# Kernel optimization log

Hardware: AMD Instinct MI355X
Metric: run time of the kernel (lower is better)

## Reference

```python
import jax, jax.numpy as jnp
import numpy as np

B, N, HID = 4, 16384, 512
H, M = 8, 32          # num_heads, num_slices
D = HID // H          # head_dim = 64


def setup_inputs() -> dict:
    key = jax.random.key(0)
    ks = jax.random.split(key, 8)
    std = 0.02
    return {
        "x": jax.random.normal(ks[0], (B, N, HID), jnp.float32),
        # Linear weights stored as [in, out] (y = x @ W + b)
        "wkv_w": jax.random.normal(ks[1], (HID, 2 * HID), jnp.float32) * std,
        "wkv_b": jnp.zeros((2 * HID,), jnp.float32),
        "wtq": jax.random.normal(ks[2], (H, M, D), jnp.float32) * std,
        "alpha": jnp.ones((H,), jnp.float32),
        "qkv_w": jax.random.normal(ks[3], (HID, 3 * HID), jnp.float32) * std,
        "out_w": jax.random.normal(ks[4], (HID, HID), jnp.float32) * std,
        "out_b": jnp.zeros((HID,), jnp.float32),
    }


def _split_heads(t):  # [b, n, h*d] -> [b, h, n, d]
    b, n, _ = t.shape
    return t.reshape(b, n, H, D).transpose(0, 2, 1, 3)


def _mha(q, k, v):
    scale = q.shape[-1] ** -0.5
    dots = jnp.einsum('bhqd,bhkd->bhqk', q, k) * scale
    attn = jax.nn.softmax(dots, axis=-1)
    out = jnp.einsum('bhqk,bhkd->bhqd', attn, v)
    return out, attn


def reference(x, wkv_w, wkv_b, wtq, alpha, qkv_w, out_w, out_b):
    kv = x @ wkv_w + wkv_b                      # [b, n, 2*hid]
    xk, xv = kv[..., :HID], kv[..., HID:]
    xk = _split_heads(xk)                       # [b, h, n, d]
    xv = _split_heads(xv)

    # slot/slice cross-attention: softmax over the slice axis m (axis=-2)
    slice_scores = jnp.einsum('hmd,bhnd->bhmn', wtq, xk)
    slice_weights = jax.nn.softmax(slice_scores * alpha[None, :, None, None], axis=-2)
    slice_token = jnp.einsum('bhmn,bhnd->bhmd', slice_weights, xv)
    slice_token = slice_token / (slice_weights.sum(axis=-1, keepdims=True) + 1e-5)
    slice_token = slice_token.transpose(0, 2, 1, 3).reshape(B, M, HID)  # b m (h d)

    # small inner MHA over the m=32 slices
    qkv = slice_token @ qkv_w                   # [b, m, 3*hid]
    q_t = _split_heads(qkv[..., :HID])
    k_t = _split_heads(qkv[..., HID:2 * HID])
    v_t = _split_heads(qkv[..., 2 * HID:])
    out_token, attn_weights = _mha(q_t, k_t, v_t)

    # scatter slice outputs back to n positions
    out = jnp.einsum('bhmd,bhmn->bhnd', out_token, slice_weights)
    out = out.transpose(0, 2, 1, 3).reshape(B, N, HID)  # b n (h d)
    out = out @ out_w + out_b
    return out, slice_weights, alpha, jnp.zeros((H, M), jnp.float32), attn_weights
```

## Files before the change

### kernel.cpp

```cpp
#include <hip/hip_runtime.h>

#define B_ 4
#define N_ 16384
#define HID_ 512
#define H_ 8
#define M_ 32
#define D_ 64

typedef __attribute__((ext_vector_type(8))) short short8;
typedef __attribute__((ext_vector_type(4))) float f32x4;

__device__ __forceinline__ short f2bf(float f) {
    unsigned u = __float_as_uint(f);
    u += 0x7fffu + ((u >> 16) & 1u);
    return (short)(u >> 16);
}
__device__ __forceinline__ float bf2f(short s) {
    return __uint_as_float(((unsigned)(unsigned short)s) << 16);
}
__device__ __forceinline__ unsigned pack2(float a, float b) {
    return (unsigned)(unsigned short)f2bf(a) | ((unsigned)(unsigned short)f2bf(b) << 16);
}
__device__ __forceinline__ void gl_lds16(const short* g, short* l) {
    __builtin_amdgcn_global_load_lds((const __attribute__((address_space(1))) unsigned*)g,
                                     (__attribute__((address_space(3))) unsigned*)l, 16, 0, 0);
}

__global__ void k_misc(const float* __restrict__ alpha, float* __restrict__ a_out,
                       float* __restrict__ z_out, const float* __restrict__ wtq,
                       short* __restrict__ wtq_bf) {
    int i = blockIdx.x * 256 + threadIdx.x;
    wtq_bf[i] = f2bf(wtq[i]);
    if (blockIdx.x == 0) {
        int t = threadIdx.x;
        if (t < H_) a_out[t] = alpha[t];
        z_out[t] = 0.f;
    }
}

__global__ void k_cvt(const float* __restrict__ src, short* __restrict__ dst) {
    int i = blockIdx.x * 256 + threadIdx.x;
    const f32x4* s = (const f32x4*)(src) + (size_t)i * 2;
    f32x4 a = s[0], b = s[1];
    short8 o;
    o[0] = f2bf(a[0]); o[1] = f2bf(a[1]); o[2] = f2bf(a[2]); o[3] = f2bf(a[3]);
    o[4] = f2bf(b[0]); o[5] = f2bf(b[1]); o[6] = f2bf(b[2]); o[7] = f2bf(b[3]);
    ((short8*)dst)[i] = o;
}

__global__ __launch_bounds__(256)
void k_wt(const float* __restrict__ w, short* __restrict__ wt) {
    __shared__ float ls[64][65];
    const int t = threadIdx.x;
    const int n0 = blockIdx.x * 64, k0 = blockIdx.y * 64;
#pragma unroll
    for (int p = 0; p < 16; ++p) {
        int idx = p * 256 + t;
        int kk = idx >> 6, nn = idx & 63;
        ls[kk][nn] = w[(size_t)(k0 + kk) * 1024 + n0 + nn];
    }
    __syncthreads();
#pragma unroll
    for (int p = 0; p < 16; ++p) {
        int idx = p * 256 + t;
        int nn = idx >> 6, kk = idx & 63;
        wt[(size_t)(n0 + nn) * 512 + k0 + kk] = f2bf(ls[kk][nn]);
    }
}

template <bool OUT_BF16>
__global__ __launch_bounds__(256, 2)
void mfma_gemm(const short* __restrict__ A, const short* __restrict__ Bt,
               const float* __restrict__ bias, void* __restrict__ Cv,
               int K, int Ncols, int b_stride, int rows_per_b, int lgx) {
    __shared__ short As[128 * 32];
    __shared__ short Bs[128 * 32];
    const int t = threadIdx.x;
    const int nwg = gridDim.x * gridDim.y;
    int id = blockIdx.y * gridDim.x + blockIdx.x;
    id = (id & 7) * (nwg >> 3) + (id >> 3);
    const int col0 = (id & ((1 << lgx) - 1)) * 128;
    const int row0 = (id >> lgx) * 128;
    const short* Bblk = Bt;
    if (b_stride) Bblk += (size_t)(row0 / rows_per_b) * (size_t)b_stride;

    const int r_a = t >> 2;
    const int c_a = (t & 3) << 3;
    const short* Ap = A + (size_t)(row0 + r_a) * K + c_a;
    const short* Bp = Bblk + (size_t)(col0 + r_a) * K + c_a;
    short* As0 = &As[t << 3];
    short* Bs0 = &Bs[t << 3];
    const size_t rowskip = (size_t)64 * K;

    const int w = t >> 6;
    const int L = t & 63;
    const int wm = (w >> 1) << 6;
    const int wn = (w & 1) << 6;
    const int lm = L & 15;
    const int lq = L >> 4;

    f32x4 acc[4][4];
#pragma unroll
    for (int i = 0; i < 4; ++i)
#pragma unroll
        for (int j = 0; j < 4; ++j) acc[i][j] = (f32x4){0.f, 0.f, 0.f, 0.f};

    for (int k0 = 0; k0 < K; k0 += 32) {
        gl_lds16(Ap + k0, As0);
        gl_lds16(Ap + k0 + rowskip, As0 + 2048);
        gl_lds16(Bp + k0, Bs0);
        gl_lds16(Bp + k0 + rowskip, Bs0 + 2048);
        __syncthreads();
        short8 af[4], bfr[4];
#pragma unroll
        for (int i = 0; i < 4; ++i)
            af[i] = *(const short8*)&As[((wm + (i << 4) + lm) << 5) + (lq << 3)];
#pragma unroll
        for (int j = 0; j < 4; ++j)
            bfr[j] = *(const short8*)&Bs[((wn + (j << 4) + lm) << 5) + (lq << 3)];
#pragma unroll
        for (int i = 0; i < 4; ++i)
#pragma unroll
            for (int j = 0; j < 4; ++j)
                acc[i][j] = __builtin_amdgcn_mfma_f32_16x16x32_bf16(af[i], bfr[j], acc[i][j], 0, 0, 0);
        __syncthreads();
    }
#pragma unroll
    for (int i = 0; i < 4; ++i) {
#pragma unroll
        for (int j = 0; j < 4; ++j) {
            const int gr = row0 + wm + (i << 4) + (lq << 2);
            const int gc = col0 + wn + (j << 4) + lm;
            const float bv = bias[gc];
#pragma unroll
            for (int r = 0; r < 4; ++r) {
                float v = acc[i][j][r] + bv;
                if constexpr (OUT_BF16)
                    ((short*)Cv)[(size_t)(gr + r) * Ncols + gc] = f2bf(v);
                else
                    ((float*)Cv)[(size_t)(gr + r) * Ncols + gc] = v;
            }
        }
    }
}

__global__ __launch_bounds__(256, 4)
void k_score(const short* __restrict__ kv, const short* __restrict__ wtq_bf,
             const float* __restrict__ alpha, float* __restrict__ sw_out,
             float* __restrict__ pws) {
    const int t = threadIdx.x;
    const int bx = blockIdx.x;
    const int chunk = bx & 63;
    const int h = (bx >> 6) & 7;
    const int b = bx >> 9;
    const int w = t >> 6;
    const int L = t & 63;
    const int lm = L & 15;
    const int g = L >> 4;
    const int n0 = chunk * 256;
    const size_t rowb = (size_t)(b * N_ + n0);
    const float al = alpha[h];

    short8 bq[2][2];
    const short* wq = wtq_bf + h * (M_ * D_);
#pragma unroll
    for (int mt = 0; mt < 2; ++mt)
#pragma unroll
        for (int ks = 0; ks < 2; ++ks)
            bq[mt][ks] = *(const short8*)(wq + (mt * 16 + lm) * 64 + ks * 32 + g * 8);

    f32x4 s[4][2];
#pragma unroll
    for (int nt = 0; nt < 4; ++nt)
#pragma unroll
        for (int mt = 0; mt < 2; ++mt) s[nt][mt] = (f32x4){0.f, 0.f, 0.f, 0.f};
#pragma unroll
    for (int ks = 0; ks < 2; ++ks) {
        short8 aq[4];
#pragma unroll
        for (int nt = 0; nt < 4; ++nt)
            aq[nt] = *(const short8*)(kv + (rowb + w * 64 + nt * 16 + lm) * 1024 +
                                      h * 64 + ks * 32 + g * 8);
#pragma unroll
        for (int nt = 0; nt < 4; ++nt)
#pragma unroll
            for (int mt = 0; mt < 2; ++mt)
                s[nt][mt] = __builtin_amdgcn_mfma_f32_16x16x32_bf16(aq[nt], bq[mt][ks], s[nt][mt], 0, 0, 0);
    }

#pragma unroll
    for (int nt = 0; nt < 4; ++nt)
#pragma unroll
        for (int r = 0; r < 4; ++r) {
            float v0 = s[nt][0][r] * al, v1 = s[nt][1][r] * al;
            float mx = fmaxf(v0, v1);
#pragma unroll
            for (int d2 = 1; d2 < 16; d2 <<= 1) mx = fmaxf(mx, __shfl_xor(mx, d2));
            float e0 = __expf(v0 - mx), e1 = __expf(v1 - mx);
            float sm = e0 + e1;
#pragma unroll
            for (int d2 = 1; d2 < 16; d2 <<= 1) sm += __shfl_xor(sm, d2);
            float inv = 1.f / sm;
            s[nt][0][r] = e0 * inv;
            s[nt][1][r] = e1 * inv;
        }

    float ws0 = 0.f, ws1 = 0.f;
#pragma unroll
    for (int nt = 0; nt < 4; ++nt) {
        const int nn = w * 64 + nt * 16 + g * 4;
#pragma unroll
        for (int mt = 0; mt < 2; ++mt) {
            const int m = mt * 16 + lm;
            *(f32x4*)(sw_out + ((size_t)((b * 8 + h) * 32 + m)) * N_ + n0 + nn) = s[nt][mt];
            float w4 = s[nt][mt][0] + s[nt][mt][1] + s[nt][mt][2] + s[nt][mt][3];
            if (mt == 0) ws0 += w4; else ws1 += w4;
        }
    }
    ws0 += __shfl_xor(ws0, 16); ws0 += __shfl_xor(ws0, 32);
    ws1 += __shfl_xor(ws1, 16); ws1 += __shfl_xor(ws1, 32);
    if (L < 16) {
        float* pw = pws + (((size_t)((b * 8 + h) * 64 + chunk)) * 4 + w) * 32;
        pw[lm] = ws0;
        pw[16 + lm] = ws1;
    }
}

__global__ __attribute__((amdgpu_flat_work_group_size(256, 256), amdgpu_waves_per_eu(3, 3)))
void k_wsum(const short* __restrict__ kv, const float* __restrict__ sw_out,
            short* __restrict__ swT, float* __restrict__ pnum) {
    __shared__ __attribute__((aligned(16))) short wT_s[M_ * 256];
    __shared__ __attribute__((aligned(16))) short xvT_s[D_ * 256];
    const int t = threadIdx.x;
    const int bx = blockIdx.x;
    const int chunk = bx & 63;
    const int h = (bx >> 6) & 7;
    const int b = bx >> 9;
    const int w = t >> 6;
    const int L = t & 63;
    const int lm = L & 15;
    const int g = L >> 4;
    const int n0 = chunk * 256;
    const size_t rowb = (size_t)(b * N_ + n0);

    short8 xv8[8];
    const short8* xvp = (const short8*)(kv + (rowb + t) * 1024 + HID_ + h * 64);
#pragma unroll
    for (int i = 0; i < 8; ++i) xv8[i] = xvp[i];

    {
        const int m = t >> 3, i = t & 7;
        const int xr = (m & 7) << 3;
        const float* rp = sw_out + ((size_t)((b * 8 + h) * 32 + m)) * N_ + n0 + i * 32;
#pragma unroll
        for (int q = 0; q < 4; ++q) {
            f32x4 a = ((const f32x4*)rp)[2 * q];
            f32x4 c = ((const f32x4*)rp)[2 * q + 1];
            int nn = i * 32 + q * 8;
            short8 v;
            v[0] = f2bf(a[0]); v[1] = f2bf(a[1]); v[2] = f2bf(a[2]); v[3] = f2bf(a[3]);
            v[4] = f2bf(c[0]); v[5] = f2bf(c[1]); v[6] = f2bf(c[2]); v[7] = f2bf(c[3]);
            *(short8*)(wT_s + m * 256 + (nn ^ xr)) = v;
        }
    }

#pragma unroll
    for (int i = 0; i < 8; ++i)
#pragma unroll
        for (int j = 0; j < 8; ++j)
            xvT_s[(i * 8 + j) * 256 + (t ^ (j << 3))] = xv8[i][j];

    __syncthreads();

    const int dcol = w * 16 + lm;
    f32x4 acc2[2];
    acc2[0] = (f32x4){0.f, 0.f, 0.f, 0.f};
    acc2[1] = (f32x4){0.f, 0.f, 0.f, 0.f};
#pragma unroll
    for (int ks = 0; ks < 8; ++ks) {
        const int kb = ks * 32 + g * 8;
        short8 bv = *(const short8*)(xvT_s + dcol * 256 + (kb ^ ((lm & 7) << 3)));
#pragma unroll
        for (int mt = 0; mt < 2; ++mt) {
            const int m = mt * 16 + lm;
            short8 av = *(const short8*)(wT_s + m * 256 + (kb ^ ((lm & 7) << 3)));
            acc2[mt] = __builtin_amdgcn_mfma_f32_16x16x32_bf16(av, bv, acc2[mt], 0, 0, 0);
        }
    }

    {
        unsigned pk[16];
#pragma unroll
        for (int mp = 0; mp < 16; ++mp) {
            unsigned a0 = (unsigned short)wT_s[(2 * mp) * 256 + (t ^ (((2 * mp) & 7) << 3))];
            unsigned a1 = (unsigned short)wT_s[(2 * mp + 1) * 256 + (t ^ (((2 * mp + 1) & 7) << 3))];
            pk[mp] = a0 | (a1 << 16);
        }
        short8* swtp = (short8*)(swT + (rowb + t) * 256 + h * 32);
#pragma unroll
        for (int q = 0; q < 4; ++q) {
            short8 v;
            v[0] = (short)(pk[4 * q] & 0xffff);     v[1] = (short)(pk[4 * q] >> 16);
            v[2] = (short)(pk[4 * q + 1] & 0xffff); v[3] = (short)(pk[4 * q + 1] >> 16);
            v[4] = (short)(pk[4 * q + 2] & 0xffff); v[5] = (short)(pk[4 * q + 2] >> 16);
            v[6] = (short)(pk[4 * q + 3] & 0xffff); v[7] = (short)(pk[4 * q + 3] >> 16);
            swtp[q] = v;
        }
    }

    float* pn = pnum + ((size_t)((b * 8 + h) * 64 + chunk)) * 2048;
#pragma unroll
    for (int mt = 0; mt < 2; ++mt)
#pragma unroll
        for (int r = 0; r < 4; ++r)
            pn[(mt * 16 + g * 4 + r) * 64 + dcol] = acc2[mt][r];
}

__global__ __launch_bounds__(256)
void k_reduce(const float* __restrict__ pnum, const float* __restrict__ pws,
              float* __restrict__ num, float* __restrict__ wsum) {
    const int bid = blockIdx.x, t = threadIdx.x;
    if (bid < 256) {
        int e = bid * 256 + t;
        int bh = e >> 11, md = e & 2047;
        const float* p = pnum + (size_t)bh * 64 * 2048 + md;
        float s = 0.f;
#pragma unroll 4
        for (int c = 0; c < 64; ++c) s += p[c * 2048];
        num[e] = s;
    } else {
        int e = (bid - 256) * 256 + t;
        int bh = e >> 5, m = e & 31;
        const float* p = pws + (size_t)bh * 64 * 4 * 32 + m;
        float s = 0.f;
#pragma unroll 4
        for (int cw = 0; cw < 256; ++cw) s += p[cw * 32];
        wsum[e] = s;
    }
}

__global__ __launch_bounds__(256, 2)
void k_qkv(const float* __restrict__ num, const float* __restrict__ wsum,
           const float* __restrict__ qkv_w, float* __restrict__ qkv) {
    __shared__ float st_s[512 * 32];
    const int t = threadIdx.x;
    const int b = blockIdx.y;
    for (int p = 0; p < 64; ++p) {
        int idx = p * 256 + t;
        int m = idx & 31, k = idx >> 5;
        int h = k >> 6, d = k & 63;
        float wsv = wsum[(b * H_ + h) * M_ + m];
        st_s[k * 32 + m] = num[((size_t)(b * H_ + h) * M_ + m) * 64 + d] / (wsv + 1e-5f);
    }
    __syncthreads();
    const int m = t >> 3;
    const int c0 = blockIdx.x * 64 + (t & 7) * 8;
    float acc[8] = {};
    for (int k = 0; k < 512; ++k) {
        float sv = st_s[k * 32 + m];
        const f32x4* wp = (const f32x4*)(qkv_w + (size_t)k * 1536 + c0);
        f32x4 w0 = wp[0], w1 = wp[1];
        acc[0] += sv * w0[0]; acc[1] += sv * w0[1]; acc[2] += sv * w0[2]; acc[3] += sv * w0[3];
        acc[4] += sv * w1[0]; acc[5] += sv * w1[1]; acc[6] += sv * w1[2]; acc[7] += sv * w1[3];
    }
    float* dst = qkv + (size_t)(b * M_ + m) * 1536 + c0;
#pragma unroll
    for (int i = 0; i < 8; ++i) dst[i] = acc[i];
}

__global__ __launch_bounds__(256)
void k_mha(const float* __restrict__ qkv, float* __restrict__ attn_out,
           float* __restrict__ ot) {
    __shared__ float q_s[32 * 65], k_s[32 * 65], v_s[32 * 65];
    __shared__ float s_s[32 * 33], p_s[32 * 33];
    const int bx = blockIdx.x;
    const int b = bx >> 3, h = bx & 7;
    const int t = threadIdx.x;
    for (int p = 0; p < 8; ++p) {
        int idx = p * 256 + t;
        int m = idx >> 6, d = idx & 63;
        size_t base = (size_t)(b * M_ + m) * 1536 + h * 64 + d;
        q_s[m * 65 + d] = qkv[base];
        k_s[m * 65 + d] = qkv[base + 512];
        v_s[m * 65 + d] = qkv[base + 1024];
    }
    __syncthreads();
    for (int p = 0; p < 4; ++p) {
        int c = p * 256 + t;
        int m = c >> 5, mm = c & 31;
        float a = 0.f;
#pragma unroll
        for (int d = 0; d < 64; ++d) a += q_s[m * 65 + d] * k_s[mm * 65 + d];
        s_s[m * 33 + mm] = a * 0.125f;
    }
    __syncthreads();
    if (t < 32) {
        float mx = -1e30f;
        for (int mm = 0; mm < 32; ++mm) mx = fmaxf(mx, s_s[t * 33 + mm]);
        float sum = 0.f;
        for (int mm = 0; mm < 32; ++mm) {
            float e = __expf(s_s[t * 33 + mm] - mx);
            p_s[t * 33 + mm] = e;
            sum += e;
        }
        float inv = 1.f / sum;
        for (int mm = 0; mm < 32; ++mm) {
            float av = p_s[t * 33 + mm] * inv;
            p_s[t * 33 + mm] = av;
            attn_out[((size_t)(b * H_ + h) * M_ + t) * M_ + mm] = av;
        }
    }
    __syncthreads();
    const int m = t >> 3, d0 = (t & 7) * 8;
    float acc[8] = {};
    for (int mm = 0; mm < 32; ++mm) {
        float av = p_s[m * 33 + mm];
#pragma unroll
        for (int j = 0; j < 8; ++j) acc[j] += av * v_s[mm * 65 + d0 + j];
    }
    float* dst = ot + ((size_t)(b * H_ + h) * M_ + m) * 64 + d0;
#pragma unroll
    for (int j = 0; j < 8; ++j) dst[j] = acc[j];
}

__global__ __launch_bounds__(256)
void k_p(const float* __restrict__ ot, const float* __restrict__ out_w,
         short* __restrict__ Pt) {
    __shared__ float ot_s[32 * 65];
    const int bh = blockIdx.y;
    const int b = bh >> 3, h = bh & 7;
    const int t = threadIdx.x;
    for (int p = 0; p < 8; ++p) {
        int idx = p * 256 + t;
        int m = idx >> 6, d = idx & 63;
        ot_s[m * 65 + d] = ot[(size_t)bh * (M_ * 64) + idx];
    }
    __syncthreads();
    const int j = blockIdx.x * 128 + (t & 127);
    const int mh = (t >> 7) * 16;
    float acc[16] = {};
    for (int d = 0; d < 64; ++d) {
        float ow = out_w[(size_t)(h * 64 + d) * HID_ + j];
#pragma unroll
        for (int i = 0; i < 16; ++i) acc[i] += ot_s[(mh + i) * 65 + d] * ow;
    }
    short* dst = Pt + ((size_t)b * HID_ + j) * (H_ * M_) + h * M_ + mh;
#pragma unroll
    for (int i = 0; i < 16; i += 2) *(unsigned*)(dst + i) = pack2(acc[i], acc[i + 1]);
}

extern "C" void kernel_launch(void* const* d_in, const int* in_sizes, int n_in,
                              void* d_out, int out_size, void* d_ws, size_t ws_size,
                              hipStream_t stream) {
    const float* x     = (const float*)d_in[0];
    const float* wkv_w = (const float*)d_in[1];
    const float* wkv_b = (const float*)d_in[2];
    const float* wtq   = (const float*)d_in[3];
    const float* alpha = (const float*)d_in[4];
    const float* qkv_w = (const float*)d_in[5];
    const float* out_w = (const float*)d_in[6];
    const float* out_b = (const float*)d_in[7];

    float* out       = (float*)d_out;
    float* sw_out    = out + (size_t)B_ * N_ * HID_;
    float* alpha_out = sw_out + (size_t)B_ * H_ * M_ * N_;
    float* zeros_out = alpha_out + H_;
    float* attn_out  = zeros_out + H_ * M_;

    short* x_bf = (short*)sw_out;
    float* pnum = out;
    float* pws  = out + 4194304;

    char* ws = (char*)d_ws;
    short* kv   = (short*)(ws);
    short* swT  = (short*)(ws + 134217728);
    short* wkvT = (short*)(ws + 167772160);
    short* Pt   = (short*)(ws + 168820736);
    float* num  = (float*)(ws + 169869312);
    float* wsum = (float*)(ws + 170131456);
    float* qkvb = (float*)(ws + 170135552);
    float* ot   = (float*)(ws + 170921984);
    short* wtq_bf = (short*)(ws + 170921984);

    k_misc<<<64, 256, 0, stream>>>(alpha, alpha_out, zeros_out, wtq, wtq_bf);
    k_cvt<<<16384, 256, 0, stream>>>(x, x_bf);
    k_wt<<<dim3(16, 8), 256, 0, stream>>>(wkv_w, wkvT);
    mfma_gemm<true><<<dim3(8, 512), 256, 0, stream>>>(
        x_bf, wkvT, wkv_b, (void*)kv, 512, 1024, 0, 1 << 30, 3);
    k_score<<<2048, 256, 0, stream>>>(kv, wtq_bf, alpha, sw_out, pws);
    k_wsum<<<2048, 256, 0, stream>>>(kv, sw_out, swT, pnum);
    k_reduce<<<260, 256, 0, stream>>>(pnum, pws, num, wsum);
    k_qkv<<<dim3(24, 4), 256, 0, stream>>>(num, wsum, qkv_w, qkvb);
    k_mha<<<32, 256, 0, stream>>>(qkvb, attn_out, ot);
    k_p<<<dim3(4, 32), 256, 0, stream>>>(ot, out_w, Pt);
    mfma_gemm<false><<<dim3(4, 512), 256, 0, stream>>>(
        swT, Pt, out_b, (void*)out, 256, 512, 131072, 16384, 2);
}
```

Baseline: 571.5 us.

## Fuse slice-score softmax into KV projection GEMM epilogue, drop K materialization

New measurement: 607.2 us. 1.06x slower.

```diff
diff --git a/kernel.cpp b/kernel.cpp
--- a/kernel.cpp
+++ b/kernel.cpp
@@ -68,6 +68,172 @@
     }
 }
 
+__global__ __launch_bounds__(256, 2)
+void k_kv(const short* __restrict__ A, const short* __restrict__ Bt,
+          const float* __restrict__ bias, const short* __restrict__ wtq_bf,
+          const float* __restrict__ alpha, short* __restrict__ vout,
+          float* __restrict__ sw_out, float* __restrict__ pws) {
+    __shared__ short As[128 * 32];
+    __shared__ short Bs[128 * 32];
+    __shared__ short Ss[128 * 128];
+    const int t = threadIdx.x;
+    int id = blockIdx.y * 8 + blockIdx.x;
+    id = (id & 7) * 512 + (id >> 3);
+    const int xb = id & 7;
+    const int row0 = (id >> 3) * 128;
+    const int col0 = xb * 128;
+    const int K = 512;
+
+    const int r_a = t >> 2;
+    const int c_a = (t & 3) << 3;
+    const short* Ap = A + (size_t)(row0 + r_a) * K + c_a;
+    const short* Bp = Bt + (size_t)(col0 + r_a) * K + c_a;
+    short* As0 = &As[t << 3];
+    short* Bs0 = &Bs[t << 3];
+    const size_t rowskip = (size_t)64 * K;
+
+    const int w = t >> 6;
+    const int L = t & 63;
+    const int wm = (w >> 1) << 6;
+    const int wn = (w & 1) << 6;
+    const int lm = L & 15;
+    const int lq = L >> 4;
+
+    f32x4 acc[4][4];
+#pragma unroll
+    for (int i = 0; i < 4; ++i)
+#pragma unroll
+        for (int j = 0; j < 4; ++j) acc[i][j] = (f32x4){0.f, 0.f, 0.f, 0.f};
+
+    for (int k0 = 0; k0 < K; k0 += 32) {
+        gl_lds16(Ap + k0, As0);
+        gl_lds16(Ap + k0 + rowskip, As0 + 2048);
+        gl_lds16(Bp + k0, Bs0);
+        gl_lds16(Bp + k0 + rowskip, Bs0 + 2048);
+        __syncthreads();
+        short8 af[4], bfr[4];
+#pragma unroll
+        for (int i = 0; i < 4; ++i)
+            af[i] = *(const short8*)&As[((wm + (i << 4) + lm) << 5) + (lq << 3)];
+#pragma unroll
+        for (int j = 0; j < 4; ++j)
+            bfr[j] = *(const short8*)&Bs[((wn + (j << 4) + lm) << 5) + (lq << 3)];
+#pragma unroll
+        for (int i = 0; i < 4; ++i)
+#pragma unroll
+            for (int j = 0; j < 4; ++j)
+                acc[i][j] = __builtin_amdgcn_mfma_f32_16x16x32_bf16(af[i], bfr[j], acc[i][j], 0, 0, 0);
+        __syncthreads();
+    }
+
+    if (xb >= 4) {
+        const int vc0 = col0 - 512;
+#pragma unroll
+        for (int i = 0; i < 4; ++i) {
+#pragma unroll
+            for (int j = 0; j < 4; ++j) {
+                const int gr = row0 + wm + (i << 4) + (lq << 2);
+                const int cl = wn + (j << 4) + lm;
+                const float bv = bias[col0 + cl];
+#pragma unroll
+                for (int r = 0; r < 4; ++r)
+                    vout[(size_t)(gr + r) * 512 + vc0 + cl] = f2bf(acc[i][j][r] + bv);
+            }
+        }
+        return;
+    }
+
+#pragma unroll
+    for (int i = 0; i < 4; ++i) {
+#pragma unroll
+        for (int j = 0; j < 4; ++j) {
+            const int cl = wn + (j << 4) + lm;
+            const float bv = bias[col0 + cl];
+#pragma unroll
+            for (int r = 0; r < 4; ++r) {
+                const int tok = wm + (i << 4) + (lq << 2) + r;
+                Ss[tok * 128 + (cl ^ ((tok & 7) << 3))] = f2bf(acc[i][j][r] + bv);
+            }
+        }
+    }
+    __syncthreads();
+
+    const int b = row0 >> 14;
+    const int nb = row0 & 16383;
+    const int panel = nb >> 7;
+    const int g = lq;
+#pragma unroll
+    for (int hh = 0; hh < 2; ++hh) {
+        const int hg = 2 * xb + hh;
+        const float al = alpha[hg];
+        const short* wq = wtq_bf + hg * (M_ * D_);
+        short8 bq[2][2];
+#pragma unroll
+        for (int mt = 0; mt < 2; ++mt)
+#pragma unroll
+            for (int ks = 0; ks < 2; ++ks)
+                bq[mt][ks] = *(const short8*)(wq + (mt * 16 + lm) * 64 + ks * 32 + g * 8);
+
+        f32x4 sc[2][2];
+#pragma unroll
+        for (int nt = 0; nt < 2; ++nt)
+#pragma unroll
+            for (int mt = 0; mt < 2; ++mt) sc[nt][mt] = (f32x4){0.f, 0.f, 0.f, 0.f};
+#pragma unroll
+        for (int ks = 0; ks < 2; ++ks) {
+            short8 aq[2];
+#pragma unroll
+            for (int nt = 0; nt < 2; ++nt) {
+                const int tok = w * 32 + nt * 16 + lm;
+                const int chan = hh * 64 + ks * 32 + g * 8;
+                aq[nt] = *(const short8*)&Ss[tok * 128 + (chan ^ ((tok & 7) << 3))];
+            }
+#pragma unroll
+            for (int nt = 0; nt < 2; ++nt)
+#pragma unroll
+                for (int mt = 0; mt < 2; ++mt)
+                    sc[nt][mt] = __builtin_amdgcn_mfma_f32_16x16x32_bf16(aq[nt], bq[mt][ks], sc[nt][mt], 0, 0, 0);
+        }
+
+#pragma unroll
+        for (int nt = 0; nt < 2; ++nt)
+#pragma unroll
+            for (int r = 0; r < 4; ++r) {
+                float v0 = sc[nt][0][r] * al, v1 = sc[nt][1][r] * al;
+                float mx = fmaxf(v0, v1);
+#pragma unroll
+                for (int d2 = 1; d2 < 16; d2 <<= 1) mx = fmaxf(mx, __shfl_xor(mx, d2));
+                float e0 = __expf(v0 - mx), e1 = __expf(v1 - mx);
+                float sm = e0 + e1;
+#pragma unroll
+                for (int d2 = 1; d2 < 16; d2 <<= 1) sm += __shfl_xor(sm, d2);
+                float inv = 1.f / sm;
+                sc[nt][0][r] = e0 * inv;
+                sc[nt][1][r] = e1 * inv;
+            }
+
+        float ws0 = 0.f, ws1 = 0.f;
+#pragma unroll
+        for (int nt = 0; nt < 2; ++nt) {
+            const int nn = nb + w * 32 + nt * 16 + g * 4;
+#pragma unroll
+            for (int mt = 0; mt < 2; ++mt) {
+                const int m = mt * 16 + lm;
+                *(f32x4*)(sw_out + ((size_t)((b * 8 + hg) * 32 + m)) * N_ + nn) = sc[nt][mt];
+                float w4 = sc[nt][mt][0] + sc[nt][mt][1] + sc[nt][mt][2] + sc[nt][mt][3];
+                if (mt == 0) ws0 += w4; else ws1 += w4;
+            }
+        }
+        ws0 += __shfl_xor(ws0, 16); ws0 += __shfl_xor(ws0, 32);
+        ws1 += __shfl_xor(ws1, 16); ws1 += __shfl_xor(ws1, 32);
+        if (L < 16) {
+            float* pw = pws + (((size_t)((b * 8 + hg) * 128 + panel)) * 4 + w) * 32;
+            pw[lm] = ws0;
+            pw[16 + lm] = ws1;
+        }
+    }
+}
+
 template <bool OUT_BF16>
 __global__ __launch_bounds__(256, 2)
 void mfma_gemm(const short* __restrict__ A, const short* __restrict__ Bt,
@@ -144,10 +310,11 @@
     }
 }
 
-__global__ __launch_bounds__(256, 4)
-void k_score(const short* __restrict__ kv, const short* __restrict__ wtq_bf,
-             const float* __restrict__ alpha, float* __restrict__ sw_out,
-             float* __restrict__ pws) {
+__global__ __attribute__((amdgpu_flat_work_group_size(256, 256), amdgpu_waves_per_eu(3, 3)))
+void k_wsum(const short* __restrict__ v, const float* __restrict__ sw_out,
+            short* __restrict__ swT, float* __restrict__ pnum) {
+    __shared__ __attribute__((aligned(16))) short wT_s[M_ * 256];
+    __shared__ __attribute__((aligned(16))) short xvT_s[D_ * 256];
     const int t = threadIdx.x;
     const int bx = blockIdx.x;
     const int chunk = bx & 63;
@@ -159,92 +326,9 @@
     const int g = L >> 4;
     const int n0 = chunk * 256;
     const size_t rowb = (size_t)(b * N_ + n0);
-    const float al = alpha[h];
-
-    short8 bq[2][2];
-    const short* wq = wtq_bf + h * (M_ * D_);
-#pragma unroll
-    for (int mt = 0; mt < 2; ++mt)
-#pragma unroll
-        for (int ks = 0; ks < 2; ++ks)
-            bq[mt][ks] = *(const short8*)(wq + (mt * 16 + lm) * 64 + ks * 32 + g * 8);
-
-    f32x4 s[4][2];
-#pragma unroll
-    for (int nt = 0; nt < 4; ++nt)
-#pragma unroll
-        for (int mt = 0; mt < 2; ++mt) s[nt][mt] = (f32x4){0.f, 0.f, 0.f, 0.f};
-#pragma unroll
-    for (int ks = 0; ks < 2; ++ks) {
-        short8 aq[4];
-#pragma unroll
-        for (int nt = 0; nt < 4; ++nt)
-            aq[nt] = *(const short8*)(kv + (rowb + w * 64 + nt * 16 + lm) * 1024 +
-                                      h * 64 + ks * 32 + g * 8);
-#pragma unroll
-        for (int nt = 0; nt < 4; ++nt)
-#pragma unroll
-            for (int mt = 0; mt < 2; ++mt)
-                s[nt][mt] = __builtin_amdgcn_mfma_f32_16x16x32_bf16(aq[nt], bq[mt][ks], s[nt][mt], 0, 0, 0);
-    }
-
-#pragma unroll
-    for (int nt = 0; nt < 4; ++nt)
-#pragma unroll
-        for (int r = 0; r < 4; ++r) {
-            float v0 = s[nt][0][r] * al, v1 = s[nt][1][r] * al;
-            float mx = fmaxf(v0, v1);
-#pragma unroll
-            for (int d2 = 1; d2 < 16; d2 <<= 1) mx = fmaxf(mx, __shfl_xor(mx, d2));
-            float e0 = __expf(v0 - mx), e1 = __expf(v1 - mx);
-            float sm = e0 + e1;
-#pragma unroll
-            for (int d2 = 1; d2 < 16; d2 <<= 1) sm += __shfl_xor(sm, d2);
-            float inv = 1.f / sm;
-            s[nt][0][r] = e0 * inv;
-            s[nt][1][r] = e1 * inv;
-        }
-
-    float ws0 = 0.f, ws1 = 0.f;
-#pragma unroll
-    for (int nt = 0; nt < 4; ++nt) {
-        const int nn = w * 64 + nt * 16 + g * 4;
-#pragma unroll
-        for (int mt = 0; mt < 2; ++mt) {
-            const int m = mt * 16 + lm;
-            *(f32x4*)(sw_out + ((size_t)((b * 8 + h) * 32 + m)) * N_ + n0 + nn) = s[nt][mt];
-            float w4 = s[nt][mt][0] + s[nt][mt][1] + s[nt][mt][2] + s[nt][mt][3];
-            if (mt == 0) ws0 += w4; else ws1 += w4;
-        }
-    }
-    ws0 += __shfl_xor(ws0, 16); ws0 += __shfl_xor(ws0, 32);
-    ws1 += __shfl_xor(ws1, 16); ws1 += __shfl_xor(ws1, 32);
-    if (L < 16) {
-        float* pw = pws + (((size_t)((b * 8 + h) * 64 + chunk)) * 4 + w) * 32;
-        pw[lm] = ws0;
-        pw[16 + lm] = ws1;
-    }
-}
-
-__global__ __attribute__((amdgpu_flat_work_group_size(256, 256), amdgpu_waves_per_eu(3, 3)))
-void k_wsum(const short* __restrict__ kv, const float* __restrict__ sw_out,
-            short* __restrict__ swT, float* __restrict__ pnum) {
-    __shared__ __attribute__((aligned(16))) short wT_s[M_ * 256];
-    __shared__ __attribute__((aligned(16))) short xvT_s[D_ * 256];
-    const int t = threadIdx.x;
-    const int bx = blockIdx.x;
-    const int chunk = bx & 63;
-    const int h = (bx >> 6) & 7;
-    const int b = bx >> 9;
-    const int w = t >> 6;
-    const int L = t & 63;
-    const int lm = L & 15;
-    const int g = L >> 4;
-    const int n0 = chunk * 256;
-    const size_t rowb = (size_t)(b * N_ + n0);
 
     short8 xv8[8];
-    const short8* xvp = (const short8*)(kv + (rowb + t) * 1024 + HID_ + h * 64);
+    const short8* xvp = (const short8*)(v + (rowb + t) * 512 + h * 64);
 #pragma unroll
     for (int i = 0; i < 8; ++i) xv8[i] = xvp[i];
 
@@ -257,10 +341,10 @@
             f32x4 a = ((const f32x4*)rp)[2 * q];
             f32x4 c = ((const f32x4*)rp)[2 * q + 1];
             int nn = i * 32 + q * 8;
-            short8 v;
-            v[0] = f2bf(a[0]); v[1] = f2bf(a[1]); v[2] = f2bf(a[2]); v[3] = f2bf(a[3]);
-            v[4] = f2bf(c[0]); v[5] = f2bf(c[1]); v[6] = f2bf(c[2]); v[7] = f2bf(c[3]);
-            *(short8*)(wT_s + m * 256 + (nn ^ xr)) = v;
+            short8 vv;
+            vv[0] = f2bf(a[0]); vv[1] = f2bf(a[1]); vv[2] = f2bf(a[2]); vv[3] = f2bf(a[3]);
+            vv[4] = f2bf(c[0]); vv[5] = f2bf(c[1]); vv[6] = f2bf(c[2]); vv[7] = f2bf(c[3]);
+            *(short8*)(wT_s + m * 256 + (nn ^ xr)) = vv;
         }
     }
 
@@ -299,12 +383,12 @@
         short8* swtp = (short8*)(swT + (rowb + t) * 256 + h * 32);
 #pragma unroll
         for (int q = 0; q < 4; ++q) {
-            short8 v;
-            v[0] = (short)(pk[4 * q] & 0xffff);     v[1] = (short)(pk[4 * q] >> 16);
-            v[2] = (short)(pk[4 * q + 1] & 0xffff); v[3] = (short)(pk[4 * q + 1] >> 16);
-            v[4] = (short)(pk[4 * q + 2] & 0xffff); v[5] = (short)(pk[4 * q + 2] >> 16);
-            v[6] = (short)(pk[4 * q + 3] & 0xffff); v[7] = (short)(pk[4 * q + 3] >> 16);
-            swtp[q] = v;
+            short8 vv;
+            vv[0] = (short)(pk[4 * q] & 0xffff);     vv[1] = (short)(pk[4 * q] >> 16);
+            vv[2] = (short)(pk[4 * q + 1] & 0xffff); vv[3] = (short)(pk[4 * q + 1] >> 16);
+            vv[4] = (short)(pk[4 * q + 2] & 0xffff); vv[5] = (short)(pk[4 * q + 2] >> 16);
+            vv[6] = (short)(pk[4 * q + 3] & 0xffff); vv[7] = (short)(pk[4 * q + 3] >> 16);
+            swtp[q] = vv;
         }
     }
 
@@ -331,10 +415,10 @@
     } else {
         int e = (bid - 256) * 256 + t;
         int bh = e >> 5, m = e & 31;
-        const float* p = pws + (size_t)bh * 64 * 4 * 32 + m;
+        const float* p = pws + (size_t)bh * (128 * 4 * 32) + m;
         float s = 0.f;
 #pragma unroll 4
-        for (int cw = 0; cw < 256; ++cw) s += p[cw * 32];
+        for (int cw = 0; cw < 512; ++cw) s += p[cw * 32];
         wsum[e] = s;
     }
 }
@@ -467,12 +551,12 @@
     float* zeros_out = alpha_out + H_;
     float* attn_out  = zeros_out + H_ * M_;
 
-    short* x_bf = (short*)sw_out;
     float* pnum = out;
     float* pws  = out + 4194304;
 
     char* ws = (char*)d_ws;
-    short* kv   = (short*)(ws);
+    short* v    = (short*)(ws);
+    short* x_bf = (short*)(ws + 67108864);
     short* swT  = (short*)(ws + 134217728);
     short* wkvT = (short*)(ws + 167772160);
     short* Pt   = (short*)(ws + 168820736);
@@ -485,10 +569,9 @@
     k_misc<<<64, 256, 0, stream>>>(alpha, alpha_out, zeros_out, wtq, wtq_bf);
     k_cvt<<<16384, 256, 0, stream>>>(x, x_bf);
     k_wt<<<dim3(16, 8), 256, 0, stream>>>(wkv_w, wkvT);
-    mfma_gemm<true><<<dim3(8, 512), 256, 0, stream>>>(
-        x_bf, wkvT, wkv_b, (void*)kv, 512, 1024, 0, 1 << 30, 3);
-    k_score<<<2048, 256, 0, stream>>>(kv, wtq_bf, alpha, sw_out, pws);
-    k_wsum<<<2048, 256, 0, stream>>>(kv, sw_out, swT, pnum);
+    k_kv<<<dim3(8, 512), 256, 0, stream>>>(
+        x_bf, wkvT, wkv_b, wtq_bf, alpha, v, sw_out, pws);
+    k_wsum<<<2048, 256, 0, stream>>>(v, sw_out, swT, pnum);
     k_reduce<<<260, 256, 0, stream>>>(pnum, pws, num, wsum);
     k_qkv<<<dim3(24, 4), 256, 0, stream>>>(num, wsum, qkv_w, qkvb);
     k_mha<<<32, 256, 0, stream>>>(qkvb, attn_out, ot);
```
